# Kernel tuning notes

Measured on AMD Instinct MI355X. Metric: run time of the kernel, lower is better.

## Reference

```python
import jax, jax.numpy as jnp
import numpy as np
import math

TOP_K = 10  # top-k codes kept by SOHO_Pre_VD for negative sampling
EPS_LN = 1e-5


def layer_norm(x, w, b):
    mu = jnp.mean(x, axis=-1, keepdims=True)
    var = jnp.mean((x - mu) ** 2, axis=-1, keepdims=True)
    return (x - mu) * jax.lax.rsqrt(var + EPS_LN) * w + b


def position_encoding_sine(b, l, d):
    # mask is all-ones [b, l]; identical across batch, compute once and broadcast
    h = w = int(math.sqrt(l))
    ones = jnp.ones((h, w), jnp.float32)
    y_embed = jnp.cumsum(ones, axis=0)
    x_embed = jnp.cumsum(ones, axis=1)
    eps = 1e-6
    two_pi = 2.0 * np.pi
    y_embed = y_embed / (y_embed[-1:, :] + eps) * two_pi
    x_embed = x_embed / (x_embed[:, -1:] + eps) * two_pi
    pf = d // 2
    dim_t = jnp.arange(pf, dtype=jnp.float32)
    dim_t = 10000.0 ** (2.0 * jnp.floor(dim_t / 2.0) / pf)
    px = x_embed[:, :, None] / dim_t  # [h, w, pf]
    py = y_embed[:, :, None] / dim_t
    # interleave sin(even), cos(odd)
    px = jnp.stack([jnp.sin(px[..., 0::2]), jnp.cos(px[..., 1::2])], axis=-1).reshape(h, w, pf)
    py = jnp.stack([jnp.sin(py[..., 0::2]), jnp.cos(py[..., 1::2])], axis=-1).reshape(h, w, pf)
    pos = jnp.concatenate([py, px], axis=-1).reshape(l, d)  # [l, d]
    return jnp.broadcast_to(pos, (b, l, d))


def setup_inputs() -> dict:
    key = jax.random.key(0)
    ks = jax.random.split(key, 10)
    B, L, CIN, D, K = 16, 576, 1024, 768, 8192
    s = 0.02
    return {
        "img": jax.random.normal(ks[0], (B, L, CIN), jnp.float32),
        "mask_indices": jax.random.randint(ks[1], (B, 1), 0, L),
        "lin_w": jax.random.normal(ks[2], (D, CIN), jnp.float32) * s,
        "lin_b": jnp.zeros((D,), jnp.float32),
        "ln1_w": jnp.ones((D,), jnp.float32),
        "ln1_b": jnp.zeros((D,), jnp.float32),
        "embed": jax.random.normal(ks[3], (K, D), jnp.float32),
        "pos_w": jax.random.normal(ks[4], (D, D), jnp.float32) * s,
        "pos_b": jnp.zeros((D,), jnp.float32),
        "gate_w": jax.random.normal(ks[5], (2, 2 * D), jnp.float32) * s,
        "gate_b": jnp.zeros((2,), jnp.float32),
        "gate_ln_w": jnp.ones((2,), jnp.float32),
        "gate_ln_b": jnp.zeros((2,), jnp.float32),
        "out_ln_w": jnp.ones((D,), jnp.float32),
        "out_ln_b": jnp.zeros((D,), jnp.float32),
    }


def reference(img, mask_indices, lin_w, lin_b, ln1_w, ln1_b, embed, pos_w, pos_b,
              gate_w, gate_b, gate_ln_w, gate_ln_b, out_ln_w, out_ln_b):
    b, l, _ = img.shape
    d = lin_w.shape[0]
    # self.linear: Linear -> LayerNorm -> ReLU
    xq = jax.nn.relu(layer_norm(img @ lin_w.T + lin_b, ln1_w, ln1_b))  # [b,l,d]
    x = xq.reshape(b * l, d)
    # SOHO VQ: nearest code by L2, straight-through
    d2 = (x * x).sum(-1, keepdims=True) - 2.0 * (x @ embed.T) + (embed * embed).sum(-1)  # [N,K]
    idx = jnp.argmin(d2, axis=-1)  # [N]
    quant = jnp.take(embed, idx, axis=0)
    quantized = x + jax.lax.stop_gradient(quant - x)
    probs = jax.nn.softmax(-d2, axis=-1)
    topk_values, topk_indices = jax.lax.top_k(probs, TOP_K)  # [N,K'],[N,K']
    # pos_align linear
    quantized = quantized @ pos_w.T + pos_b
    emb_pt = quantized.reshape(b, l, d)
    # gated fusion
    g = jnp.concatenate([emb_pt, xq], axis=-1) @ gate_w.T + gate_b  # [b,l,2]
    g = jax.nn.relu(layer_norm(g, gate_ln_w, gate_ln_b))
    score = jax.nn.softmax(g, axis=-1)
    emb_s, img_s = score[..., 0:1], score[..., 1:2]
    emb_pt = emb_pt * emb_s + xq * img_s
    pos = position_encoding_sine(b, l, d)
    # negative index construction (visual_mask is all ones)
    ind = idx.reshape(b, l).astype(jnp.float32)  # [b,l]
    masked_labels = jnp.take_along_axis(ind, mask_indices, axis=1)  # [b,1]
    masked_neg = (ind == masked_labels).astype(jnp.float32)[..., None]  # [b,l,1]
    samp = jax.random.categorical(jax.random.key(42), jnp.log(topk_values))  # [N]
    neg = jnp.take_along_axis(topk_indices, samp[:, None], axis=1).reshape(b, l, 1).astype(jnp.float32)
    neg_at_mask = jnp.take_along_axis(neg[..., 0], mask_indices, axis=1)[..., None]  # [b,1,1]
    neg_idx = neg_at_mask * masked_neg + ind[..., None] * (1.0 - masked_neg)  # [b,l,1]
    neg_idx = neg_idx.reshape(b * l).astype(jnp.int32)
    # one-hot matmul == embedding gather
    neg_q = jnp.take(embed, neg_idx, axis=0).reshape(b, l, d)
    neg_q = neg_q * emb_s + jax.lax.stop_gradient(xq) * img_s
    out_pos = layer_norm(emb_pt + pos, out_ln_w, out_ln_b)
    out_neg = layer_norm(neg_q + pos, out_ln_w, out_ln_b)
    return (out_pos, out_neg)
```

## Files before the change

kernel.cpp:

```cpp
#include <hip/hip_runtime.h>
#include <stdint.h>

#define M_TOT  9216
#define D_     768
#define CIN_   1024
#define KCODE  8192
#define TOPK   10

typedef unsigned short u16;
typedef __bf16 bf16x8 __attribute__((ext_vector_type(8)));
typedef float f32x4 __attribute__((ext_vector_type(4)));


__device__ inline float block_sum(float v, float* red) {
    int t = threadIdx.x;
    red[t] = v;
    __syncthreads();
    #pragma unroll
    for (int s = 128; s > 0; s >>= 1) {
        if (t < s) red[t] += red[t + s];
        __syncthreads();
    }
    float r = red[0];
    __syncthreads();
    return r;
}

__device__ inline unsigned long long umin64(unsigned long long a, unsigned long long b) {
    return (a < b) ? a : b;
}

__device__ inline u16 f2bf(float f) {
    uint32_t u = __float_as_uint(f);
    uint32_t r = (u + 0x7fffu + ((u >> 16) & 1u)) >> 16;
    return (u16)r;
}
__device__ inline float bf2f(u16 h) {
    return __uint_as_float(((uint32_t)h) << 16);
}

__device__ inline unsigned long long shfl_xor_u64(unsigned long long v, int mask) {
    int lo = (int)(uint32_t)v, hi = (int)(uint32_t)(v >> 32);
    lo = __shfl_xor(lo, mask, 64);
    hi = __shfl_xor(hi, mask, 64);
    return ((unsigned long long)(uint32_t)hi << 32) | (uint32_t)lo;
}

#define GLDS(gp, lp) __builtin_amdgcn_global_load_lds( \
    (const __attribute__((address_space(1))) unsigned int*)(gp), \
    (__attribute__((address_space(3))) unsigned int*)(lp), 16, 0, 0)

__global__ __launch_bounds__(256) void k_split3(const float* __restrict__ in,
    u16* __restrict__ h, u16* __restrict__ m, u16* __restrict__ l, int n4)
{
    int i = blockIdx.x * 256 + threadIdx.x;
    int stride = gridDim.x * 256;
    for (; i < n4; i += stride) {
        float4 v = ((const float4*)in)[i];
        ushort4 hv, mv, lv;
        float x, r;
        x = v.x; hv.x = f2bf(x); r = x - bf2f(hv.x); mv.x = f2bf(r); lv.x = f2bf(r - bf2f(mv.x));
        x = v.y; hv.y = f2bf(x); r = x - bf2f(hv.y); mv.y = f2bf(r); lv.y = f2bf(r - bf2f(mv.y));
        x = v.z; hv.z = f2bf(x); r = x - bf2f(hv.z); mv.z = f2bf(r); lv.z = f2bf(r - bf2f(mv.z));
        x = v.w; hv.w = f2bf(x); r = x - bf2f(hv.w); mv.w = f2bf(r); lv.w = f2bf(r - bf2f(mv.w));
        ((ushort4*)h)[i] = hv; ((ushort4*)m)[i] = mv; ((ushort4*)l)[i] = lv;
    }
}

__global__ __launch_bounds__(256) void k_split2(const float* __restrict__ in,
    u16* __restrict__ h, u16* __restrict__ l, int n4)
{
    int i = blockIdx.x * 256 + threadIdx.x;
    int stride = gridDim.x * 256;
    for (; i < n4; i += stride) {
        float4 v = ((const float4*)in)[i];
        ushort4 hv, lv;
        hv.x = f2bf(v.x); lv.x = f2bf(v.x - bf2f(hv.x));
        hv.y = f2bf(v.y); lv.y = f2bf(v.y - bf2f(hv.y));
        hv.z = f2bf(v.z); lv.z = f2bf(v.z - bf2f(hv.z));
        hv.w = f2bf(v.w); lv.w = f2bf(v.w - bf2f(hv.w));
        ((ushort4*)h)[i] = hv; ((ushort4*)l)[i] = lv;
    }
}

__global__ __launch_bounds__(256) void k_gemm1_mfma(
    const u16* __restrict__ Ah, const u16* __restrict__ Am, const u16* __restrict__ Al,
    const u16* __restrict__ Bh, const u16* __restrict__ Bm, const u16* __restrict__ Bl,
    const float* __restrict__ bias, float* __restrict__ C)
{
    __shared__ __align__(16) u16 sm[24576];
    const int t = threadIdx.x;
    const int lane = t & 63, wid = t >> 6;
    const int row0 = blockIdx.y * 128, col0 = blockIdx.x * 128;
    const int r16 = lane & 15, kb = lane >> 4;
    const int wr = wid >> 1, wc = wid & 1;
    const int sc = (lane & 3) * 8;
    const int lrow = lane >> 2;

    f32x4 acc[4][4];
    #pragma unroll
    for (int mf = 0; mf < 4; ++mf)
        #pragma unroll
        for (int nf = 0; nf < 4; ++nf)
            acc[mf][nf] = (f32x4){0.f, 0.f, 0.f, 0.f};

    for (int k0 = 0; k0 < CIN_; k0 += 32) {
        __syncthreads();
        #pragma unroll
        for (int i = 0; i < 12; ++i) {
            int mat = i >> 1;
            int c = (i & 1) ? wid + 4 : wid;
            const u16* mp = (mat == 0) ? Ah : (mat == 1) ? Am : (mat == 2) ? Al
                          : (mat == 3) ? Bh : (mat == 4) ? Bm : Bl;
            int rbase = (mat < 3) ? row0 : col0;
            const u16* g = mp + (size_t)(rbase + c * 16 + lrow) * CIN_ + k0 + sc;
            GLDS(g, sm + mat * 4096 + c * 512);
        }
        __syncthreads();

        bf16x8 bh[4], bm[4], bl[4];
        #pragma unroll
        for (int nf = 0; nf < 4; ++nf) {
            int offb = 12288 + (wc * 64 + nf * 16 + r16) * 32 + kb * 8;
            bh[nf] = *(const bf16x8*)(sm + offb);
            bm[nf] = *(const bf16x8*)(sm + offb + 4096);
            bl[nf] = *(const bf16x8*)(sm + offb + 8192);
        }
        #pragma unroll
        for (int mf = 0; mf < 4; ++mf) {
            int offa = (wr * 64 + mf * 16 + r16) * 32 + kb * 8;
            bf16x8 ah = *(const bf16x8*)(sm + offa);
            bf16x8 am = *(const bf16x8*)(sm + offa + 4096);
            bf16x8 al = *(const bf16x8*)(sm + offa + 8192);
            #pragma unroll
            for (int nf = 0; nf < 4; ++nf) {
                acc[mf][nf] = __builtin_amdgcn_mfma_f32_16x16x32_bf16(ah, bh[nf], acc[mf][nf], 0, 0, 0);
                acc[mf][nf] = __builtin_amdgcn_mfma_f32_16x16x32_bf16(ah, bm[nf], acc[mf][nf], 0, 0, 0);
                acc[mf][nf] = __builtin_amdgcn_mfma_f32_16x16x32_bf16(am, bh[nf], acc[mf][nf], 0, 0, 0);
                acc[mf][nf] = __builtin_amdgcn_mfma_f32_16x16x32_bf16(am, bm[nf], acc[mf][nf], 0, 0, 0);
                acc[mf][nf] = __builtin_amdgcn_mfma_f32_16x16x32_bf16(ah, bl[nf], acc[mf][nf], 0, 0, 0);
                acc[mf][nf] = __builtin_amdgcn_mfma_f32_16x16x32_bf16(al, bh[nf], acc[mf][nf], 0, 0, 0);
            }
        }
    }

    #pragma unroll
    for (int mf = 0; mf < 4; ++mf) {
        #pragma unroll
        for (int q = 0; q < 4; ++q) {
            int m = row0 + wr * 64 + mf * 16 + kb * 4 + q;
            #pragma unroll
            for (int nf = 0; nf < 4; ++nf) {
                int n = col0 + wc * 64 + nf * 16 + r16;
                C[(size_t)m * D_ + n] = acc[mf][nf][q] + bias[n];
            }
        }
    }
}

__global__ __launch_bounds__(256) void k_gemm3_mfma(
    const u16* __restrict__ Eh, const u16* __restrict__ El,
    const u16* __restrict__ Ph, const u16* __restrict__ Pl,
    const int* __restrict__ gather,
    const float* __restrict__ bias, float* __restrict__ C)
{
    __shared__ __align__(16) u16 sm[16384];
    const int t = threadIdx.x;
    const int lane = t & 63, wid = t >> 6;
    const int row0 = blockIdx.y * 128, col0 = blockIdx.x * 128;
    const int r16 = lane & 15, kb = lane >> 4;
    const int wr = wid >> 1, wc = wid & 1;
    const int sc = (lane & 3) * 8;
    const int lrow = lane >> 2;

    int gi0 = gather[row0 + wid * 16 + lrow];
    int gi1 = gather[row0 + (wid + 4) * 16 + lrow];

    f32x4 acc[4][4];
    #pragma unroll
    for (int mf = 0; mf < 4; ++mf)
        #pragma unroll
        for (int nf = 0; nf < 4; ++nf)
            acc[mf][nf] = (f32x4){0.f, 0.f, 0.f, 0.f};

    for (int k0 = 0; k0 < D_; k0 += 32) {
        __syncthreads();
        #pragma unroll
        for (int i = 0; i < 8; ++i) {
            int mat = i >> 1;
            int c = (i & 1) ? wid + 4 : wid;
            int grow = (i & 1) ? gi1 : gi0;
            const u16* g;
            if (mat == 0)      g = Eh + (size_t)grow * D_ + k0 + sc;
            else if (mat == 1) g = El + (size_t)grow * D_ + k0 + sc;
            else if (mat == 2) g = Ph + (size_t)(col0 + c * 16 + lrow) * D_ + k0 + sc;
            else               g = Pl + (size_t)(col0 + c * 16 + lrow) * D_ + k0 + sc;
            GLDS(g, sm + mat * 4096 + c * 512);
        }
        __syncthreads();

        bf16x8 bh[4], bl[4];
        #pragma unroll
        for (int nf = 0; nf < 4; ++nf) {
            int offb = 8192 + (wc * 64 + nf * 16 + r16) * 32 + kb * 8;
            bh[nf] = *(const bf16x8*)(sm + offb);
            bl[nf] = *(const bf16x8*)(sm + offb + 4096);
        }
        #pragma unroll
        for (int mf = 0; mf < 4; ++mf) {
            int offa = (wr * 64 + mf * 16 + r16) * 32 + kb * 8;
            bf16x8 ah = *(const bf16x8*)(sm + offa);
            bf16x8 al = *(const bf16x8*)(sm + offa + 4096);
            #pragma unroll
            for (int nf = 0; nf < 4; ++nf) {
                acc[mf][nf] = __builtin_amdgcn_mfma_f32_16x16x32_bf16(ah, bh[nf], acc[mf][nf], 0, 0, 0);
                acc[mf][nf] = __builtin_amdgcn_mfma_f32_16x16x32_bf16(ah, bl[nf], acc[mf][nf], 0, 0, 0);
                acc[mf][nf] = __builtin_amdgcn_mfma_f32_16x16x32_bf16(al, bh[nf], acc[mf][nf], 0, 0, 0);
            }
        }
    }

    #pragma unroll
    for (int mf = 0; mf < 4; ++mf) {
        #pragma unroll
        for (int q = 0; q < 4; ++q) {
            int m = row0 + wr * 64 + mf * 16 + kb * 4 + q;
            #pragma unroll
            for (int nf = 0; nf < 4; ++nf) {
                int n = col0 + wc * 64 + nf * 16 + r16;
                C[(size_t)m * D_ + n] = acc[mf][nf][q] + bias[n];
            }
        }
    }
}

__global__ __launch_bounds__(256) void k_gemm2_mfma(
    const u16* __restrict__ Xh, const u16* __restrict__ Xl,
    const u16* __restrict__ Eh, const u16* __restrict__ El,
    const float* __restrict__ xsq, const float* __restrict__ esq,
    unsigned long long* __restrict__ amin)
{
    __shared__ __align__(16) u16 sm[16384];
    const int t = threadIdx.x;
    const int lane = t & 63, wid = t >> 6;
    const int row0 = blockIdx.y * 128, col0 = blockIdx.x * 128;
    const int r16 = lane & 15, kb = lane >> 4;
    const int wr = wid >> 1, wc = wid & 1;

    f32x4 acc[4][4];
    #pragma unroll
    for (int mf = 0; mf < 4; ++mf)
        #pragma unroll
        for (int nf = 0; nf < 4; ++nf)
            acc[mf][nf] = (f32x4){0.f, 0.f, 0.f, 0.f};

    const u16* sb = (wid == 0) ? Xh : (wid == 1) ? Xl : (wid == 2) ? Eh : El;
    const int rbase = (wid < 2) ? row0 : col0;
    const int srow = rbase + (lane >> 2);
    const int scol = (lane & 3) * 8;
    u16* ldsw = sm + wid * 4096;

    for (int k0 = 0; k0 < D_; k0 += 32) {
        __syncthreads();
        #pragma unroll
        for (int c = 0; c < 8; ++c) {
            const u16* g = sb + (size_t)(srow + c * 16) * D_ + k0 + scol;
            GLDS(g, ldsw + c * 512);
        }
        __syncthreads();

        bf16x8 bh[4], bl[4];
        #pragma unroll
        for (int nf = 0; nf < 4; ++nf) {
            int offb = 8192 + (wc * 64 + nf * 16 + r16) * 32 + kb * 8;
            bh[nf] = *(const bf16x8*)(sm + offb);
            bl[nf] = *(const bf16x8*)(sm + offb + 4096);
        }
        #pragma unroll
        for (int mf = 0; mf < 4; ++mf) {
            int offa = (wr * 64 + mf * 16 + r16) * 32 + kb * 8;
            bf16x8 ah = *(const bf16x8*)(sm + offa);
            bf16x8 al = *(const bf16x8*)(sm + offa + 4096);
            #pragma unroll
            for (int nf = 0; nf < 4; ++nf) {
                acc[mf][nf] = __builtin_amdgcn_mfma_f32_16x16x32_bf16(ah, bh[nf], acc[mf][nf], 0, 0, 0);
                acc[mf][nf] = __builtin_amdgcn_mfma_f32_16x16x32_bf16(ah, bl[nf], acc[mf][nf], 0, 0, 0);
                acc[mf][nf] = __builtin_amdgcn_mfma_f32_16x16x32_bf16(al, bh[nf], acc[mf][nf], 0, 0, 0);
            }
        }
    }

    float esqv[4];
    #pragma unroll
    for (int nf = 0; nf < 4; ++nf)
        esqv[nf] = esq[col0 + wc * 64 + nf * 16 + r16];

    #pragma unroll
    for (int mf = 0; mf < 4; ++mf) {
        #pragma unroll
        for (int q = 0; q < 4; ++q) {
            int m = row0 + wr * 64 + mf * 16 + kb * 4 + q;
            float xsv = xsq[m];
            unsigned long long best = ~0ull;
            #pragma unroll
            for (int nf = 0; nf < 4; ++nf) {
                int n = col0 + wc * 64 + nf * 16 + r16;
                float d2 = (xsv - 2.0f * acc[mf][nf][q]) + esqv[nf];
                unsigned long long key =
                    ((unsigned long long)__float_as_uint(d2) << 32) | (unsigned)n;
                best = umin64(best, key);
            }
            #pragma unroll
            for (int msk = 1; msk < 16; msk <<= 1)
                best = umin64(best, shfl_xor_u64(best, msk));
            if (r16 == 0) atomicMin(&amin[m], best);
        }
    }
}

__global__ __launch_bounds__(256) void k_ln_relu(
    const float* __restrict__ in, const float* __restrict__ w,
    const float* __restrict__ b, float* __restrict__ xq, float* __restrict__ xsq,
    u16* __restrict__ Xh, u16* __restrict__ Xl)
{
    __shared__ float red[256];
    int r = blockIdx.x, t = threadIdx.x;
    const float* row = in + (size_t)r * D_;
    float v0 = row[t], v1 = row[t + 256], v2 = row[t + 512];
    float mu = block_sum(v0 + v1 + v2, red) * (1.0f / 768.0f);
    float d0 = v0 - mu, d1 = v1 - mu, d2 = v2 - mu;
    float var = block_sum(d0 * d0 + d1 * d1 + d2 * d2, red) * (1.0f / 768.0f);
    float rn = 1.0f / sqrtf(var + 1e-5f);
    float o0 = fmaxf(0.0f, d0 * rn * w[t] + b[t]);
    float o1 = fmaxf(0.0f, d1 * rn * w[t + 256] + b[t + 256]);
    float o2 = fmaxf(0.0f, d2 * rn * w[t + 512] + b[t + 512]);
    float* orow = xq + (size_t)r * D_;
    orow[t] = o0; orow[t + 256] = o1; orow[t + 512] = o2;
    u16 h0 = f2bf(o0), h1 = f2bf(o1), h2 = f2bf(o2);
    Xh[(size_t)r * D_ + t]       = h0;
    Xh[(size_t)r * D_ + t + 256] = h1;
    Xh[(size_t)r * D_ + t + 512] = h2;
    Xl[(size_t)r * D_ + t]       = f2bf(o0 - bf2f(h0));
    Xl[(size_t)r * D_ + t + 256] = f2bf(o1 - bf2f(h1));
    Xl[(size_t)r * D_ + t + 512] = f2bf(o2 - bf2f(h2));
    float q = block_sum(o0 * o0 + o1 * o1 + o2 * o2, red);
    if (t == 0) xsq[r] = q;
}

__global__ __launch_bounds__(256) void k_esq(const float* __restrict__ E,
                                             float* __restrict__ esq,
                                             u16* __restrict__ Eh,
                                             u16* __restrict__ El)
{
    __shared__ float red[256];
    int r = blockIdx.x, t = threadIdx.x;
    const float* row = E + (size_t)r * D_;
    float v0 = row[t], v1 = row[t + 256], v2 = row[t + 512];
    u16 h0 = f2bf(v0), h1 = f2bf(v1), h2 = f2bf(v2);
    Eh[(size_t)r * D_ + t]       = h0;
    Eh[(size_t)r * D_ + t + 256] = h1;
    Eh[(size_t)r * D_ + t + 512] = h2;
    El[(size_t)r * D_ + t]       = f2bf(v0 - bf2f(h0));
    El[(size_t)r * D_ + t + 256] = f2bf(v1 - bf2f(h1));
    El[(size_t)r * D_ + t + 512] = f2bf(v2 - bf2f(h2));
    float s = block_sum(v0 * v0 + v1 * v1 + v2 * v2, red);
    if (t == 0) esq[r] = s;
}

__global__ void k_extract(const unsigned long long* __restrict__ amin,
                          int* __restrict__ idx, int n)
{
    int i = blockIdx.x * 256 + threadIdx.x;
    if (i < n) idx[i] = (int)(amin[i] & 0xFFFFFFFFull);
}

__global__ __launch_bounds__(256) void k_gate(
    const float* __restrict__ embpt, const float* __restrict__ xq,
    const float* __restrict__ gw, const float* __restrict__ gb,
    const float* __restrict__ glnw, const float* __restrict__ glnb,
    float* __restrict__ scores)
{
    __shared__ float red[256];
    int r = blockIdx.x, t = threadIdx.x;
    const float* ep = embpt + (size_t)r * D_;
    const float* xr = xq + (size_t)r * D_;
    float g0 = 0.0f, g1 = 0.0f;
    for (int k = t; k < 1536; k += 256) {
        float v = (k < 768) ? ep[k] : xr[k - 768];
        g0 = fmaf(v, gw[k], g0);
        g1 = fmaf(v, gw[1536 + k], g1);
    }
    g0 = block_sum(g0, red);
    g1 = block_sum(g1, red);
    if (t == 0) {
        g0 += gb[0]; g1 += gb[1];
        float mu = 0.5f * (g0 + g1);
        float h0 = g0 - mu, h1 = g1 - mu;
        float var = 0.5f * (h0 * h0 + h1 * h1);
        float rn = 1.0f / sqrtf(var + 1e-5f);
        float o0 = fmaxf(0.0f, h0 * rn * glnw[0] + glnb[0]);
        float o1 = fmaxf(0.0f, h1 * rn * glnw[1] + glnb[1]);
        float m = fmaxf(o0, o1);
        float e0 = expf(o0 - m), e1 = expf(o1 - m);
        float inv = 1.0f / (e0 + e1);
        scores[r * 2 + 0] = e0 * inv;
        scores[r * 2 + 1] = e1 * inv;
    }
}

__global__ __launch_bounds__(256) void k_pos(float* __restrict__ pos)
{
    int l = blockIdx.x, t = threadIdx.x;
    for (int k = t; k < D_; k += 256) {
        int kk = (k < 384) ? k : k - 384;
        int m = kk >> 1;
        double coord = (k < 384) ? (double)(l / 24) : (double)(l % 24);
        double v = (coord + 1.0) / (24.0 + 1e-6) * 6.283185307179586;
        double tm = pow(10000.0, (double)m / 192.0);
        double a = v / tm;
        pos[(size_t)l * D_ + k] = (float)((kk & 1) ? cos(a) : sin(a));
    }
}

__global__ __launch_bounds__(256) void k_d2row(
    const float* __restrict__ xq, const float* __restrict__ E,
    const float* __restrict__ xsq, const float* __restrict__ esq,
    const int* __restrict__ mask, float* __restrict__ d2row)
{
    __shared__ float xs[768];
    int b = blockIdx.x;
    int g = blockIdx.y;
    int t = threadIdx.x;
    int r = b * 576 + mask[b];
    xs[t]       = xq[(size_t)r * D_ + t];
    xs[t + 256] = xq[(size_t)r * D_ + t + 256];
    xs[t + 512] = xq[(size_t)r * D_ + t + 512];
    __syncthreads();
    int lane = t & 63, w = t >> 6;
    float xsr = xsq[r];
    for (int e = 0; e < 16; ++e) {
        int j = g * 64 + w * 16 + e;
        const float* er = E + (size_t)j * D_;
        float p = 0.0f;
        for (int k = lane; k < D_; k += 64) p = fmaf(xs[k], er[k], p);
        #pragma unroll
        for (int off = 32; off > 0; off >>= 1) p += __shfl_down(p, off);
        if (lane == 0) d2row[b * KCODE + j] = (xsr - 2.0f * p) + esq[j];
    }
}

__device__ inline void threefry2x32(uint32_t x0, uint32_t x1,
                                    uint32_t& o0, uint32_t& o1)
{
    const uint32_t ks0 = 0u, ks1 = 42u;
    const uint32_t ks2 = ks0 ^ ks1 ^ 0x1BD11BDAu;
    uint32_t ks[3] = {ks0, ks1, ks2};
    x0 += ks[0]; x1 += ks[1];
    const int R0[4] = {13, 15, 26, 6};
    const int R1[4] = {17, 29, 16, 24};
    #pragma unroll
    for (int i = 0; i < 5; ++i) {
        const int* R = (i & 1) ? R1 : R0;
        #pragma unroll
        for (int q = 0; q < 4; ++q) {
            x0 += x1;
            x1 = (x1 << R[q]) | (x1 >> (32 - R[q]));
            x1 ^= x0;
        }
        x0 += ks[(i + 1) % 3];
        x1 += ks[(i + 2) % 3] + (uint32_t)(i + 1);
    }
    o0 = x0; o1 = x1;
}

__global__ __launch_bounds__(256) void k_topk_sample(
    const float* __restrict__ d2row, const unsigned long long* __restrict__ amin,
    const int* __restrict__ mask, int* __restrict__ mlabel, int* __restrict__ negsel)
{
    __shared__ float sd2[KCODE];
    __shared__ unsigned long long rbuf[256];
    __shared__ float rfs[256];
    __shared__ int sel[TOPK];
    __shared__ float selv[TOPK];
    __shared__ float sS;
    int b = blockIdx.x, t = threadIdx.x;
    for (int j = t; j < KCODE; j += 256) sd2[j] = d2row[b * KCODE + j];
    __syncthreads();
    for (int p = 0; p < TOPK; ++p) {
        unsigned long long best = ~0ull;
        for (int j = t; j < KCODE; j += 256) {
            bool skip = false;
            for (int q = 0; q < p; ++q) skip = skip || (j == sel[q]);
            if (skip) continue;
            unsigned long long key =
                ((unsigned long long)__float_as_uint(sd2[j]) << 32) | (unsigned)j;
            best = umin64(best, key);
        }
        rbuf[t] = best;
        __syncthreads();
        for (int s = 128; s > 0; s >>= 1) {
            if (t < s) rbuf[t] = umin64(rbuf[t], rbuf[t + s]);
            __syncthreads();
        }
// ... 160 lines not shown
```

Before: 880.5 us.

## Double-buffer LDS staging in split-bf16 GEMMs and switch to k-major LDS layout

The gather-GEMM and distance-GEMM kernels now use two LDS buffers, prefetching the next K tile with global_load_lds while MFMAs run on the current one. This leaves one barrier per iteration instead of two. The LDS layout of all three GEMMs changes to k-major chunks, with each lane loading a full row segment, to change access and bank patterns. The positional-encoding kernel replaces double-precision pow/sin/cos with float exp2f/sinf/cosf, trading some accuracy for cheaper math. Double buffering doubles shared memory per block, which may reduce occupancy.

```diff
diff --git a/kernel.cpp b/kernel.cpp
--- a/kernel.cpp
+++ b/kernel.cpp
@@ -50,38 +50,6 @@
     (const __attribute__((address_space(1))) unsigned int*)(gp), \
     (__attribute__((address_space(3))) unsigned int*)(lp), 16, 0, 0)
 
-__global__ __launch_bounds__(256) void k_split3(const float* __restrict__ in,
-    u16* __restrict__ h, u16* __restrict__ m, u16* __restrict__ l, int n4)
-{
-    int i = blockIdx.x * 256 + threadIdx.x;
-    int stride = gridDim.x * 256;
-    for (; i < n4; i += stride) {
-        float4 v = ((const float4*)in)[i];
-        ushort4 hv, mv, lv;
-        float x, r;
-        x = v.x; hv.x = f2bf(x); r = x - bf2f(hv.x); mv.x = f2bf(r); lv.x = f2bf(r - bf2f(mv.x));
-        x = v.y; hv.y = f2bf(x); r = x - bf2f(hv.y); mv.y = f2bf(r); lv.y = f2bf(r - bf2f(mv.y));
-        x = v.z; hv.z = f2bf(x); r = x - bf2f(hv.z); mv.z = f2bf(r); lv.z = f2bf(r - bf2f(mv.z));
-        x = v.w; hv.w = f2bf(x); r = x - bf2f(hv.w); mv.w = f2bf(r); lv.w = f2bf(r - bf2f(mv.w));
-        ((ushort4*)h)[i] = hv; ((ushort4*)m)[i] = mv; ((ushort4*)l)[i] = lv;
-    }
-}
-
-__global__ __launch_bounds__(256) void k_split2(const float* __restrict__ in,
-    u16* __restrict__ h, u16* __restrict__ l, int n4)
-{
-    int i = blockIdx.x * 256 + threadIdx.x;
-    int stride = gridDim.x * 256;
-    for (; i < n4; i += stride) {
-        float4 v = ((const float4*)in)[i];
-        ushort4 hv, lv;
-        hv.x = f2bf(v.x); lv.x = f2bf(v.x - bf2f(hv.x));
-        hv.y = f2bf(v.y); lv.y = f2bf(v.y - bf2f(hv.y));
-        hv.z = f2bf(v.z); lv.z = f2bf(v.z - bf2f(hv.z));
-        hv.w = f2bf(v.w); lv.w = f2bf(v.w - bf2f(hv.w));
-        ((ushort4*)h)[i] = hv; ((ushort4*)l)[i] = lv;
-    }
-}
 
 __global__ __launch_bounds__(256) void k_gemm1_mfma(
     const u16* __restrict__ Ah, const u16* __restrict__ Am, const u16* __restrict__ Al,
@@ -94,8 +62,6 @@
     const int row0 = blockIdx.y * 128, col0 = blockIdx.x * 128;
     const int r16 = lane & 15, kb = lane >> 4;
     const int wr = wid >> 1, wc = wid & 1;
-    const int sc = (lane & 3) * 8;
-    const int lrow = lane >> 2;
 
     f32x4 acc[4][4];
     #pragma unroll
@@ -113,7 +79,8 @@
             const u16* mp = (mat == 0) ? Ah : (mat == 1) ? Am : (mat == 2) ? Al
                           : (mat == 3) ? Bh : (mat == 4) ? Bm : Bl;
             int rbase = (mat < 3) ? row0 : col0;
-            const u16* g = mp + (size_t)(rbase + c * 16 + lrow) * CIN_ + k0 + sc;
+            const u16* g = mp + (size_t)(rbase + (c & 1) * 64 + lane) * CIN_
+                             + k0 + (c >> 1) * 8;
             GLDS(g, sm + mat * 4096 + c * 512);
         }
         __syncthreads();
@@ -121,17 +88,17 @@
         bf16x8 bh[4], bm[4], bl[4];
         #pragma unroll
         for (int nf = 0; nf < 4; ++nf) {
-            int offb = 12288 + (wc * 64 + nf * 16 + r16) * 32 + kb * 8;
-            bh[nf] = *(const bf16x8*)(sm + offb);
-            bm[nf] = *(const bf16x8*)(sm + offb + 4096);
-            bl[nf] = *(const bf16x8*)(sm + offb + 8192);
+            int off = kb * 1024 + (wc * 64 + nf * 16 + r16) * 8;
+            bh[nf] = *(const bf16x8*)(sm + 12288 + off);
+            bm[nf] = *(const bf16x8*)(sm + 16384 + off);
+            bl[nf] = *(const bf16x8*)(sm + 20480 + off);
         }
         #pragma unroll
         for (int mf = 0; mf < 4; ++mf) {
-            int offa = (wr * 64 + mf * 16 + r16) * 32 + kb * 8;
-            bf16x8 ah = *(const bf16x8*)(sm + offa);
-            bf16x8 am = *(const bf16x8*)(sm + offa + 4096);
-            bf16x8 al = *(const bf16x8*)(sm + offa + 8192);
+            int off = kb * 1024 + (wr * 64 + mf * 16 + r16) * 8;
+            bf16x8 ah = *(const bf16x8*)(sm + off);
+            bf16x8 am = *(const bf16x8*)(sm + 4096 + off);
+            bf16x8 al = *(const bf16x8*)(sm + 8192 + off);
             #pragma unroll
             for (int nf = 0; nf < 4; ++nf) {
                 acc[mf][nf] = __builtin_amdgcn_mfma_f32_16x16x32_bf16(ah, bh[nf], acc[mf][nf], 0, 0, 0);
@@ -164,17 +131,12 @@
     const int* __restrict__ gather,
     const float* __restrict__ bias, float* __restrict__ C)
 {
-    __shared__ __align__(16) u16 sm[16384];
+    __shared__ __align__(16) u16 sm[2][16384];
     const int t = threadIdx.x;
     const int lane = t & 63, wid = t >> 6;
     const int row0 = blockIdx.y * 128, col0 = blockIdx.x * 128;
     const int r16 = lane & 15, kb = lane >> 4;
     const int wr = wid >> 1, wc = wid & 1;
-    const int sc = (lane & 3) * 8;
-    const int lrow = lane >> 2;
-
-    int gi0 = gather[row0 + wid * 16 + lrow];
-    int gi1 = gather[row0 + (wid + 4) * 16 + lrow];
 
     f32x4 acc[4][4];
     #pragma unroll
@@ -183,34 +145,45 @@
         for (int nf = 0; nf < 4; ++nf)
             acc[mf][nf] = (f32x4){0.f, 0.f, 0.f, 0.f};
 
-    for (int k0 = 0; k0 < D_; k0 += 32) {
-        __syncthreads();
-        #pragma unroll
-        for (int i = 0; i < 8; ++i) {
-            int mat = i >> 1;
-            int c = (i & 1) ? wid + 4 : wid;
-            int grow = (i & 1) ? gi1 : gi0;
-            const u16* g;
-            if (mat == 0)      g = Eh + (size_t)grow * D_ + k0 + sc;
-            else if (mat == 1) g = El + (size_t)grow * D_ + k0 + sc;
-            else if (mat == 2) g = Ph + (size_t)(col0 + c * 16 + lrow) * D_ + k0 + sc;
-            else               g = Pl + (size_t)(col0 + c * 16 + lrow) * D_ + k0 + sc;
-            GLDS(g, sm + mat * 4096 + c * 512);
-        }
-        __syncthreads();
-
+    const u16* sb = (wid == 0) ? Eh : (wid == 1) ? El : (wid == 2) ? Ph : Pl;
+    int re, ro;
+    if (wid < 2) {
+        re = gather[row0 + lane];
+        ro = gather[row0 + 64 + lane];
+    } else {
+        re = col0 + lane;
+        ro = col0 + 64 + lane;
+    }
+    const u16* src0 = sb + (size_t)re * D_;
+    const u16* src1 = sb + (size_t)ro * D_;
+
+    auto STAGE = [&](int buf, int k0) {
+        u16* dst = sm[buf] + wid * 4096;
+        #pragma unroll
+        for (int c = 0; c < 8; ++c) {
+            const u16* g = ((c & 1) ? src1 : src0) + k0 + (c >> 1) * 8;
+            GLDS(g, dst + c * 512);
+        }
+    };
+
+    STAGE(0, 0);
+    __syncthreads();
+    for (int kt = 0; kt < 24; ++kt) {
+        int cur = kt & 1;
+        if (kt < 23) STAGE(cur ^ 1, (kt + 1) * 32);
+        const u16* B = sm[cur];
         bf16x8 bh[4], bl[4];
         #pragma unroll
         for (int nf = 0; nf < 4; ++nf) {
-            int offb = 8192 + (wc * 64 + nf * 16 + r16) * 32 + kb * 8;
-            bh[nf] = *(const bf16x8*)(sm + offb);
-            bl[nf] = *(const bf16x8*)(sm + offb + 4096);
+            int off = kb * 1024 + (wc * 64 + nf * 16 + r16) * 8;
+            bh[nf] = *(const bf16x8*)(B + 8192 + off);
+            bl[nf] = *(const bf16x8*)(B + 12288 + off);
         }
         #pragma unroll
         for (int mf = 0; mf < 4; ++mf) {
-            int offa = (wr * 64 + mf * 16 + r16) * 32 + kb * 8;
-            bf16x8 ah = *(const bf16x8*)(sm + offa);
-            bf16x8 al = *(const bf16x8*)(sm + offa + 4096);
+            int off = kb * 1024 + (wr * 64 + mf * 16 + r16) * 8;
+            bf16x8 ah = *(const bf16x8*)(B + off);
+            bf16x8 al = *(const bf16x8*)(B + 4096 + off);
             #pragma unroll
             for (int nf = 0; nf < 4; ++nf) {
                 acc[mf][nf] = __builtin_amdgcn_mfma_f32_16x16x32_bf16(ah, bh[nf], acc[mf][nf], 0, 0, 0);
@@ -218,6 +191,7 @@
                 acc[mf][nf] = __builtin_amdgcn_mfma_f32_16x16x32_bf16(al, bh[nf], acc[mf][nf], 0, 0, 0);
             }
         }
+        __syncthreads();
     }
 
     #pragma unroll
@@ -240,7 +214,7 @@
     const float* __restrict__ xsq, const float* __restrict__ esq,
     unsigned long long* __restrict__ amin)
 {
-    __shared__ __align__(16) u16 sm[16384];
+    __shared__ __align__(16) u16 sm[2][16384];
     const int t = threadIdx.x;
     const int lane = t & 63, wid = t >> 6;
     const int row0 = blockIdx.y * 128, col0 = blockIdx.x * 128;
@@ -256,31 +230,36 @@
 
     const u16* sb = (wid == 0) ? Xh : (wid == 1) ? Xl : (wid == 2) ? Eh : El;
     const int rbase = (wid < 2) ? row0 : col0;
-    const int srow = rbase + (lane >> 2);
-    const int scol = (lane & 3) * 8;
-    u16* ldsw = sm + wid * 4096;
-
-    for (int k0 = 0; k0 < D_; k0 += 32) {
-        __syncthreads();
+    const u16* src0 = sb + (size_t)(rbase + lane) * D_;
+    const u16* src1 = sb + (size_t)(rbase + 64 + lane) * D_;
+
+    auto STAGE = [&](int buf, int k0) {
+        u16* dst = sm[buf] + wid * 4096;
         #pragma unroll
         for (int c = 0; c < 8; ++c) {
-            const u16* g = sb + (size_t)(srow + c * 16) * D_ + k0 + scol;
-            GLDS(g, ldsw + c * 512);
-        }
-        __syncthreads();
-
+            const u16* g = ((c & 1) ? src1 : src0) + k0 + (c >> 1) * 8;
+            GLDS(g, dst + c * 512);
+        }
+    };
+
+    STAGE(0, 0);
+    __syncthreads();
+    for (int kt = 0; kt < 24; ++kt) {
+        int cur = kt & 1;
+        if (kt < 23) STAGE(cur ^ 1, (kt + 1) * 32);
+        const u16* B = sm[cur];
         bf16x8 bh[4], bl[4];
         #pragma unroll
         for (int nf = 0; nf < 4; ++nf) {
-            int offb = 8192 + (wc * 64 + nf * 16 + r16) * 32 + kb * 8;
-            bh[nf] = *(const bf16x8*)(sm + offb);
-            bl[nf] = *(const bf16x8*)(sm + offb + 4096);
+            int off = kb * 1024 + (wc * 64 + nf * 16 + r16) * 8;
+            bh[nf] = *(const bf16x8*)(B + 8192 + off);
+            bl[nf] = *(const bf16x8*)(B + 12288 + off);
         }
         #pragma unroll
         for (int mf = 0; mf < 4; ++mf) {
-            int offa = (wr * 64 + mf * 16 + r16) * 32 + kb * 8;
-            bf16x8 ah = *(const bf16x8*)(sm + offa);
-            bf16x8 al = *(const bf16x8*)(sm + offa + 4096);
+            int off = kb * 1024 + (wr * 64 + mf * 16 + r16) * 8;
+            bf16x8 ah = *(const bf16x8*)(B + off);
+            bf16x8 al = *(const bf16x8*)(B + 4096 + off);
             #pragma unroll
             for (int nf = 0; nf < 4; ++nf) {
                 acc[mf][nf] = __builtin_amdgcn_mfma_f32_16x16x32_bf16(ah, bh[nf], acc[mf][nf], 0, 0, 0);
@@ -288,6 +267,7 @@
                 acc[mf][nf] = __builtin_amdgcn_mfma_f32_16x16x32_bf16(al, bh[nf], acc[mf][nf], 0, 0, 0);
             }
         }
+        __syncthreads();
     }
 
     float esqv[4];
@@ -315,6 +295,39 @@
                 best = umin64(best, shfl_xor_u64(best, msk));
             if (r16 == 0) atomicMin(&amin[m], best);
         }
+    }
+}
+
+__global__ __launch_bounds__(256) void k_split3(const float* __restrict__ in,
+    u16* __restrict__ h, u16* __restrict__ m, u16* __restrict__ l, int n4)
+{
+    int i = blockIdx.x * 256 + threadIdx.x;
+    int stride = gridDim.x * 256;
+    for (; i < n4; i += stride) {
+        float4 v = ((const float4*)in)[i];
+        ushort4 hv, mv, lv;
+        float x, r;
+        x = v.x; hv.x = f2bf(x); r = x - bf2f(hv.x); mv.x = f2bf(r); lv.x = f2bf(r - bf2f(mv.x));
+        x = v.y; hv.y = f2bf(x); r = x - bf2f(hv.y); mv.y = f2bf(r); lv.y = f2bf(r - bf2f(mv.y));
+        x = v.z; hv.z = f2bf(x); r = x - bf2f(hv.z); mv.z = f2bf(r); lv.z = f2bf(r - bf2f(mv.z));
+        x = v.w; hv.w = f2bf(x); r = x - bf2f(hv.w); mv.w = f2bf(r); lv.w = f2bf(r - bf2f(mv.w));
+        ((ushort4*)h)[i] = hv; ((ushort4*)m)[i] = mv; ((ushort4*)l)[i] = lv;
+    }
+}
+
+__global__ __launch_bounds__(256) void k_split2(const float* __restrict__ in,
+    u16* __restrict__ h, u16* __restrict__ l, int n4)
+{
+    int i = blockIdx.x * 256 + threadIdx.x;
+    int stride = gridDim.x * 256;
+    for (; i < n4; i += stride) {
+        float4 v = ((const float4*)in)[i];
+        ushort4 hv, lv;
+        hv.x = f2bf(v.x); lv.x = f2bf(v.x - bf2f(hv.x));
+        hv.y = f2bf(v.y); lv.y = f2bf(v.y - bf2f(hv.y));
+        hv.z = f2bf(v.z); lv.z = f2bf(v.z - bf2f(hv.z));
+        hv.w = f2bf(v.w); lv.w = f2bf(v.w - bf2f(hv.w));
+        ((ushort4*)h)[i] = hv; ((ushort4*)l)[i] = lv;
     }
 }
 
@@ -414,11 +427,11 @@
     for (int k = t; k < D_; k += 256) {
         int kk = (k < 384) ? k : k - 384;
         int m = kk >> 1;
-        double coord = (k < 384) ? (double)(l / 24) : (double)(l % 24);
-        double v = (coord + 1.0) / (24.0 + 1e-6) * 6.283185307179586;
-        double tm = pow(10000.0, (double)m / 192.0);
-        double a = v / tm;
-        pos[(size_t)l * D_ + k] = (float)((kk & 1) ? cos(a) : sin(a));
+        float coord = (k < 384) ? (float)(l / 24) : (float)(l % 24);
+        float v = (coord + 1.0f) / 24.000001f * 6.28318530717958647692f;
+        float tm = exp2f((float)m * (13.287712379549449f / 192.0f));
+        float a = v / tm;
+        pos[(size_t)l * D_ + k] = (kk & 1) ? cosf(a) : sinf(a);
     }
 }
 
```

New measurement: 1.463 ms. 1.66x slower.

## Widen gemm2 K-tile to 64 with XOR-swizzled LDS and float pos encoding

Applied to the files above, without the earlier changes.

The distance GEMM kernel now stages 64-wide K slices instead of 32, in a 32K-element shared buffer. It uses an XOR-swizzled LDS layout to avoid bank conflicts and halves the number of barrier pairs per tile. The kernel definitions are also moved earlier in the file. Separately, the sine position encoding switches from double-precision pow/sin/cos to float exp2f/sinf/cosf. That is cheaper on the GPU but slightly less accurate.

```diff
diff --git a/kernel.cpp b/kernel.cpp
--- a/kernel.cpp
+++ b/kernel.cpp
@@ -49,6 +49,244 @@
 #define GLDS(gp, lp) __builtin_amdgcn_global_load_lds( \
     (const __attribute__((address_space(1))) unsigned int*)(gp), \
     (__attribute__((address_space(3))) unsigned int*)(lp), 16, 0, 0)
+
+__global__ __launch_bounds__(256) void k_gemm1_mfma(
+    const u16* __restrict__ Ah, const u16* __restrict__ Am, const u16* __restrict__ Al,
+    const u16* __restrict__ Bh, const u16* __restrict__ Bm, const u16* __restrict__ Bl,
+    const float* __restrict__ bias, float* __restrict__ C)
+{
+    __shared__ __align__(16) u16 sm[24576];
+    const int t = threadIdx.x;
+    const int lane = t & 63, wid = t >> 6;
+    const int row0 = blockIdx.y * 128, col0 = blockIdx.x * 128;
+    const int r16 = lane & 15, kb = lane >> 4;
+    const int wr = wid >> 1, wc = wid & 1;
+    const int sc = (lane & 3) * 8;
+    const int lrow = lane >> 2;
+
+    f32x4 acc[4][4];
+    #pragma unroll
+    for (int mf = 0; mf < 4; ++mf)
+        #pragma unroll
+        for (int nf = 0; nf < 4; ++nf)
+            acc[mf][nf] = (f32x4){0.f, 0.f, 0.f, 0.f};
+
+    for (int k0 = 0; k0 < CIN_; k0 += 32) {
+        __syncthreads();
+        #pragma unroll
+        for (int i = 0; i < 12; ++i) {
+            int mat = i >> 1;
+            int c = (i & 1) ? wid + 4 : wid;
+            const u16* mp = (mat == 0) ? Ah : (mat == 1) ? Am : (mat == 2) ? Al
+                          : (mat == 3) ? Bh : (mat == 4) ? Bm : Bl;
+            int rbase = (mat < 3) ? row0 : col0;
+            const u16* g = mp + (size_t)(rbase + c * 16 + lrow) * CIN_ + k0 + sc;
+            GLDS(g, sm + mat * 4096 + c * 512);
+        }
+        __syncthreads();
+
+        bf16x8 bh[4], bm[4], bl[4];
+        #pragma unroll
+        for (int nf = 0; nf < 4; ++nf) {
+            int offb = 12288 + (wc * 64 + nf * 16 + r16) * 32 + kb * 8;
+            bh[nf] = *(const bf16x8*)(sm + offb);
+            bm[nf] = *(const bf16x8*)(sm + offb + 4096);
+            bl[nf] = *(const bf16x8*)(sm + offb + 8192);
+        }
+        #pragma unroll
+        for (int mf = 0; mf < 4; ++mf) {
+            int offa = (wr * 64 + mf * 16 + r16) * 32 + kb * 8;
+            bf16x8 ah = *(const bf16x8*)(sm + offa);
+            bf16x8 am = *(const bf16x8*)(sm + offa + 4096);
+            bf16x8 al = *(const bf16x8*)(sm + offa + 8192);
+            #pragma unroll
+            for (int nf = 0; nf < 4; ++nf) {
+                acc[mf][nf] = __builtin_amdgcn_mfma_f32_16x16x32_bf16(ah, bh[nf], acc[mf][nf], 0, 0, 0);
+                acc[mf][nf] = __builtin_amdgcn_mfma_f32_16x16x32_bf16(ah, bm[nf], acc[mf][nf], 0, 0, 0);
+                acc[mf][nf] = __builtin_amdgcn_mfma_f32_16x16x32_bf16(am, bh[nf], acc[mf][nf], 0, 0, 0);
+                acc[mf][nf] = __builtin_amdgcn_mfma_f32_16x16x32_bf16(am, bm[nf], acc[mf][nf], 0, 0, 0);
+                acc[mf][nf] = __builtin_amdgcn_mfma_f32_16x16x32_bf16(ah, bl[nf], acc[mf][nf], 0, 0, 0);
+                acc[mf][nf] = __builtin_amdgcn_mfma_f32_16x16x32_bf16(al, bh[nf], acc[mf][nf], 0, 0, 0);
+            }
+        }
+    }
+
+    #pragma unroll
+    for (int mf = 0; mf < 4; ++mf) {
+        #pragma unroll
+        for (int q = 0; q < 4; ++q) {
+            int m = row0 + wr * 64 + mf * 16 + kb * 4 + q;
+            #pragma unroll
+            for (int nf = 0; nf < 4; ++nf) {
+                int n = col0 + wc * 64 + nf * 16 + r16;
+                C[(size_t)m * D_ + n] = acc[mf][nf][q] + bias[n];
+            }
+        }
+    }
+}
+
+__global__ __launch_bounds__(256) void k_gemm3_mfma(
+    const u16* __restrict__ Eh, const u16* __restrict__ El,
+    const u16* __restrict__ Ph, const u16* __restrict__ Pl,
+    const int* __restrict__ gather,
+    const float* __restrict__ bias, float* __restrict__ C)
+{
+    __shared__ __align__(16) u16 sm[16384];
+    const int t = threadIdx.x;
+    const int lane = t & 63, wid = t >> 6;
+    const int row0 = blockIdx.y * 128, col0 = blockIdx.x * 128;
+    const int r16 = lane & 15, kb = lane >> 4;
+    const int wr = wid >> 1, wc = wid & 1;
+    const int sc = (lane & 3) * 8;
+    const int lrow = lane >> 2;
+
+    int gi0 = gather[row0 + wid * 16 + lrow];
+    int gi1 = gather[row0 + (wid + 4) * 16 + lrow];
+
+    f32x4 acc[4][4];
+    #pragma unroll
+    for (int mf = 0; mf < 4; ++mf)
+        #pragma unroll
+        for (int nf = 0; nf < 4; ++nf)
+            acc[mf][nf] = (f32x4){0.f, 0.f, 0.f, 0.f};
+
+    for (int k0 = 0; k0 < D_; k0 += 32) {
+        __syncthreads();
+        #pragma unroll
+        for (int i = 0; i < 8; ++i) {
+            int mat = i >> 1;
+            int c = (i & 1) ? wid + 4 : wid;
+            int grow = (i & 1) ? gi1 : gi0;
+            const u16* g;
+            if (mat == 0)      g = Eh + (size_t)grow * D_ + k0 + sc;
+            else if (mat == 1) g = El + (size_t)grow * D_ + k0 + sc;
+            else if (mat == 2) g = Ph + (size_t)(col0 + c * 16 + lrow) * D_ + k0 + sc;
+            else               g = Pl + (size_t)(col0 + c * 16 + lrow) * D_ + k0 + sc;
+            GLDS(g, sm + mat * 4096 + c * 512);
+        }
+        __syncthreads();
+
+        bf16x8 bh[4], bl[4];
+        #pragma unroll
+        for (int nf = 0; nf < 4; ++nf) {
+            int offb = 8192 + (wc * 64 + nf * 16 + r16) * 32 + kb * 8;
+            bh[nf] = *(const bf16x8*)(sm + offb);
+            bl[nf] = *(const bf16x8*)(sm + offb + 4096);
+        }
+        #pragma unroll
+        for (int mf = 0; mf < 4; ++mf) {
+            int offa = (wr * 64 + mf * 16 + r16) * 32 + kb * 8;
+            bf16x8 ah = *(const bf16x8*)(sm + offa);
+            bf16x8 al = *(const bf16x8*)(sm + offa + 4096);
+            #pragma unroll
+            for (int nf = 0; nf < 4; ++nf) {
+                acc[mf][nf] = __builtin_amdgcn_mfma_f32_16x16x32_bf16(ah, bh[nf], acc[mf][nf], 0, 0, 0);
+                acc[mf][nf] = __builtin_amdgcn_mfma_f32_16x16x32_bf16(ah, bl[nf], acc[mf][nf], 0, 0, 0);
+                acc[mf][nf] = __builtin_amdgcn_mfma_f32_16x16x32_bf16(al, bh[nf], acc[mf][nf], 0, 0, 0);
+            }
+        }
+    }
+
+    #pragma unroll
+    for (int mf = 0; mf < 4; ++mf) {
+        #pragma unroll
+        for (int q = 0; q < 4; ++q) {
+            int m = row0 + wr * 64 + mf * 16 + kb * 4 + q;
+            #pragma unroll
+            for (int nf = 0; nf < 4; ++nf) {
+                int n = col0 + wc * 64 + nf * 16 + r16;
+                C[(size_t)m * D_ + n] = acc[mf][nf][q] + bias[n];
+            }
+        }
+    }
+}
+
+__global__ __launch_bounds__(256) void k_gemm2_mfma(
+    const u16* __restrict__ Xh, const u16* __restrict__ Xl,
+    const u16* __restrict__ Eh, const u16* __restrict__ El,
+    const float* __restrict__ xsq, const float* __restrict__ esq,
+    unsigned long long* __restrict__ amin)
+{
+    __shared__ __align__(16) u16 sm[32768];
+    const int t = threadIdx.x;
+    const int lane = t & 63, wid = t >> 6;
+    const int row0 = blockIdx.y * 128, col0 = blockIdx.x * 128;
+    const int r16 = lane & 15, kb = lane >> 4;
+    const int wr = wid >> 1, wc = wid & 1;
+
+    f32x4 acc[4][4];
+    #pragma unroll
+    for (int mf = 0; mf < 4; ++mf)
+        #pragma unroll
+        for (int nf = 0; nf < 4; ++nf)
+            acc[mf][nf] = (f32x4){0.f, 0.f, 0.f, 0.f};
+
+    const u16* sb = (wid == 0) ? Xh : (wid == 1) ? Xl : (wid == 2) ? Eh : El;
+    const int rbase = (wid < 2) ? row0 : col0;
+    const u16* srcb = sb + (size_t)(rbase + (lane >> 3)) * D_
+                         + ((lane & 7) ^ (lane >> 3)) * 8;
+    u16* dstb = sm + wid * 8192 + lane * 8;
+
+    const int swz = (r16 & 7);
+    for (int kt = 0; kt < 12; ++kt) {
+        __syncthreads();
+        #pragma unroll
+        for (int c = 0; c < 16; ++c) {
+            GLDS(srcb + kt * 64 + c * 8 * D_, dstb + c * 512);
+        }
+        __syncthreads();
+        #pragma unroll
+        for (int h = 0; h < 2; ++h) {
+            const int slot = ((h * 4 + kb) ^ swz) * 8;
+            bf16x8 bh[4], bl[4];
+            #pragma unroll
+            for (int nf = 0; nf < 4; ++nf) {
+                int off = (wc * 64 + nf * 16 + r16) * 64 + slot;
+                bh[nf] = *(const bf16x8*)(sm + 16384 + off);
+                bl[nf] = *(const bf16x8*)(sm + 24576 + off);
+            }
+            #pragma unroll
+            for (int mf = 0; mf < 4; ++mf) {
+                int off = (wr * 64 + mf * 16 + r16) * 64 + slot;
+                bf16x8 ah = *(const bf16x8*)(sm + off);
+                bf16x8 al = *(const bf16x8*)(sm + 8192 + off);
+                #pragma unroll
+                for (int nf = 0; nf < 4; ++nf) {
+                    acc[mf][nf] = __builtin_amdgcn_mfma_f32_16x16x32_bf16(ah, bh[nf], acc[mf][nf], 0, 0, 0);
+                    acc[mf][nf] = __builtin_amdgcn_mfma_f32_16x16x32_bf16(ah, bl[nf], acc[mf][nf], 0, 0, 0);
+                    acc[mf][nf] = __builtin_amdgcn_mfma_f32_16x16x32_bf16(al, bh[nf], acc[mf][nf], 0, 0, 0);
+                }
+            }
+        }
+    }
+
+    float esqv[4];
+    #pragma unroll
+    for (int nf = 0; nf < 4; ++nf)
+        esqv[nf] = esq[col0 + wc * 64 + nf * 16 + r16];
+
+    #pragma unroll
+    for (int mf = 0; mf < 4; ++mf) {
+        #pragma unroll
+        for (int q = 0; q < 4; ++q) {
+            int m = row0 + wr * 64 + mf * 16 + kb * 4 + q;
+            float xsv = xsq[m];
+            unsigned long long best = ~0ull;
+            #pragma unroll
+            for (int nf = 0; nf < 4; ++nf) {
+                int n = col0 + wc * 64 + nf * 16 + r16;
+                float d2 = (xsv - 2.0f * acc[mf][nf][q]) + esqv[nf];
+                unsigned long long key =
+                    ((unsigned long long)__float_as_uint(d2) << 32) | (unsigned)n;
+                best = umin64(best, key);
+            }
+            #pragma unroll
+            for (int msk = 1; msk < 16; msk <<= 1)
+                best = umin64(best, shfl_xor_u64(best, msk));
+            if (r16 == 0) atomicMin(&amin[m], best);
+        }
+    }
+}
 
 __global__ __launch_bounds__(256) void k_split3(const float* __restrict__ in,
     u16* __restrict__ h, u16* __restrict__ m, u16* __restrict__ l, int n4)
@@ -80,241 +318,6 @@
         hv.z = f2bf(v.z); lv.z = f2bf(v.z - bf2f(hv.z));
         hv.w = f2bf(v.w); lv.w = f2bf(v.w - bf2f(hv.w));
         ((ushort4*)h)[i] = hv; ((ushort4*)l)[i] = lv;
-    }
-}
-
-__global__ __launch_bounds__(256) void k_gemm1_mfma(
-    const u16* __restrict__ Ah, const u16* __restrict__ Am, const u16* __restrict__ Al,
-    const u16* __restrict__ Bh, const u16* __restrict__ Bm, const u16* __restrict__ Bl,
-    const float* __restrict__ bias, float* __restrict__ C)
-{
-    __shared__ __align__(16) u16 sm[24576];
-    const int t = threadIdx.x;
-    const int lane = t & 63, wid = t >> 6;
-    const int row0 = blockIdx.y * 128, col0 = blockIdx.x * 128;
-    const int r16 = lane & 15, kb = lane >> 4;
-    const int wr = wid >> 1, wc = wid & 1;
-    const int sc = (lane & 3) * 8;
-    const int lrow = lane >> 2;
-
-    f32x4 acc[4][4];
-    #pragma unroll
-    for (int mf = 0; mf < 4; ++mf)
-        #pragma unroll
-        for (int nf = 0; nf < 4; ++nf)
-            acc[mf][nf] = (f32x4){0.f, 0.f, 0.f, 0.f};
-
-    for (int k0 = 0; k0 < CIN_; k0 += 32) {
-        __syncthreads();
-        #pragma unroll
-        for (int i = 0; i < 12; ++i) {
-            int mat = i >> 1;
-            int c = (i & 1) ? wid + 4 : wid;
-            const u16* mp = (mat == 0) ? Ah : (mat == 1) ? Am : (mat == 2) ? Al
-                          : (mat == 3) ? Bh : (mat == 4) ? Bm : Bl;
-            int rbase = (mat < 3) ? row0 : col0;
-            const u16* g = mp + (size_t)(rbase + c * 16 + lrow) * CIN_ + k0 + sc;
-            GLDS(g, sm + mat * 4096 + c * 512);
-        }
-        __syncthreads();
-
-        bf16x8 bh[4], bm[4], bl[4];
-        #pragma unroll
-        for (int nf = 0; nf < 4; ++nf) {
-            int offb = 12288 + (wc * 64 + nf * 16 + r16) * 32 + kb * 8;
-            bh[nf] = *(const bf16x8*)(sm + offb);
-            bm[nf] = *(const bf16x8*)(sm + offb + 4096);
-            bl[nf] = *(const bf16x8*)(sm + offb + 8192);
-        }
-        #pragma unroll
-        for (int mf = 0; mf < 4; ++mf) {
-            int offa = (wr * 64 + mf * 16 + r16) * 32 + kb * 8;
-            bf16x8 ah = *(const bf16x8*)(sm + offa);
-            bf16x8 am = *(const bf16x8*)(sm + offa + 4096);
-            bf16x8 al = *(const bf16x8*)(sm + offa + 8192);
-            #pragma unroll
-            for (int nf = 0; nf < 4; ++nf) {
-                acc[mf][nf] = __builtin_amdgcn_mfma_f32_16x16x32_bf16(ah, bh[nf], acc[mf][nf], 0, 0, 0);
-                acc[mf][nf] = __builtin_amdgcn_mfma_f32_16x16x32_bf16(ah, bm[nf], acc[mf][nf], 0, 0, 0);
-                acc[mf][nf] = __builtin_amdgcn_mfma_f32_16x16x32_bf16(am, bh[nf], acc[mf][nf], 0, 0, 0);
-                acc[mf][nf] = __builtin_amdgcn_mfma_f32_16x16x32_bf16(am, bm[nf], acc[mf][nf], 0, 0, 0);
-                acc[mf][nf] = __builtin_amdgcn_mfma_f32_16x16x32_bf16(ah, bl[nf], acc[mf][nf], 0, 0, 0);
-                acc[mf][nf] = __builtin_amdgcn_mfma_f32_16x16x32_bf16(al, bh[nf], acc[mf][nf], 0, 0, 0);
-            }
-        }
-    }
-
-    #pragma unroll
-    for (int mf = 0; mf < 4; ++mf) {
-        #pragma unroll
-        for (int q = 0; q < 4; ++q) {
-            int m = row0 + wr * 64 + mf * 16 + kb * 4 + q;
-            #pragma unroll
-            for (int nf = 0; nf < 4; ++nf) {
-                int n = col0 + wc * 64 + nf * 16 + r16;
-                C[(size_t)m * D_ + n] = acc[mf][nf][q] + bias[n];
-            }
-        }
-    }
-}
-
-__global__ __launch_bounds__(256) void k_gemm3_mfma(
-    const u16* __restrict__ Eh, const u16* __restrict__ El,
-    const u16* __restrict__ Ph, const u16* __restrict__ Pl,
-    const int* __restrict__ gather,
-    const float* __restrict__ bias, float* __restrict__ C)
-{
-    __shared__ __align__(16) u16 sm[16384];
-    const int t = threadIdx.x;
-    const int lane = t & 63, wid = t >> 6;
-    const int row0 = blockIdx.y * 128, col0 = blockIdx.x * 128;
-    const int r16 = lane & 15, kb = lane >> 4;
-    const int wr = wid >> 1, wc = wid & 1;
-    const int sc = (lane & 3) * 8;
-    const int lrow = lane >> 2;
-
-    int gi0 = gather[row0 + wid * 16 + lrow];
-    int gi1 = gather[row0 + (wid + 4) * 16 + lrow];
-
-    f32x4 acc[4][4];
-    #pragma unroll
-    for (int mf = 0; mf < 4; ++mf)
-        #pragma unroll
-        for (int nf = 0; nf < 4; ++nf)
-            acc[mf][nf] = (f32x4){0.f, 0.f, 0.f, 0.f};
-
-    for (int k0 = 0; k0 < D_; k0 += 32) {
-        __syncthreads();
-        #pragma unroll
-        for (int i = 0; i < 8; ++i) {
-            int mat = i >> 1;
-            int c = (i & 1) ? wid + 4 : wid;
-            int grow = (i & 1) ? gi1 : gi0;
-            const u16* g;
-            if (mat == 0)      g = Eh + (size_t)grow * D_ + k0 + sc;
-            else if (mat == 1) g = El + (size_t)grow * D_ + k0 + sc;
-            else if (mat == 2) g = Ph + (size_t)(col0 + c * 16 + lrow) * D_ + k0 + sc;
-            else               g = Pl + (size_t)(col0 + c * 16 + lrow) * D_ + k0 + sc;
-            GLDS(g, sm + mat * 4096 + c * 512);
-        }
-        __syncthreads();
-
-        bf16x8 bh[4], bl[4];
-        #pragma unroll
-        for (int nf = 0; nf < 4; ++nf) {
-            int offb = 8192 + (wc * 64 + nf * 16 + r16) * 32 + kb * 8;
-            bh[nf] = *(const bf16x8*)(sm + offb);
-            bl[nf] = *(const bf16x8*)(sm + offb + 4096);
-        }
-        #pragma unroll
-        for (int mf = 0; mf < 4; ++mf) {
-            int offa = (wr * 64 + mf * 16 + r16) * 32 + kb * 8;
-            bf16x8 ah = *(const bf16x8*)(sm + offa);
-            bf16x8 al = *(const bf16x8*)(sm + offa + 4096);
-            #pragma unroll
-            for (int nf = 0; nf < 4; ++nf) {
-                acc[mf][nf] = __builtin_amdgcn_mfma_f32_16x16x32_bf16(ah, bh[nf], acc[mf][nf], 0, 0, 0);
-                acc[mf][nf] = __builtin_amdgcn_mfma_f32_16x16x32_bf16(ah, bl[nf], acc[mf][nf], 0, 0, 0);
-                acc[mf][nf] = __builtin_amdgcn_mfma_f32_16x16x32_bf16(al, bh[nf], acc[mf][nf], 0, 0, 0);
-            }
-        }
-    }
-
-    #pragma unroll
-    for (int mf = 0; mf < 4; ++mf) {
-        #pragma unroll
-        for (int q = 0; q < 4; ++q) {
-            int m = row0 + wr * 64 + mf * 16 + kb * 4 + q;
-            #pragma unroll
-            for (int nf = 0; nf < 4; ++nf) {
-                int n = col0 + wc * 64 + nf * 16 + r16;
-                C[(size_t)m * D_ + n] = acc[mf][nf][q] + bias[n];
-            }
-        }
-    }
-}
-
-__global__ __launch_bounds__(256) void k_gemm2_mfma(
-    const u16* __restrict__ Xh, const u16* __restrict__ Xl,
-    const u16* __restrict__ Eh, const u16* __restrict__ El,
-    const float* __restrict__ xsq, const float* __restrict__ esq,
-    unsigned long long* __restrict__ amin)
-{
-    __shared__ __align__(16) u16 sm[16384];
-    const int t = threadIdx.x;
-    const int lane = t & 63, wid = t >> 6;
-    const int row0 = blockIdx.y * 128, col0 = blockIdx.x * 128;
-    const int r16 = lane & 15, kb = lane >> 4;
-    const int wr = wid >> 1, wc = wid & 1;
-
-    f32x4 acc[4][4];
-    #pragma unroll
-    for (int mf = 0; mf < 4; ++mf)
-        #pragma unroll
-        for (int nf = 0; nf < 4; ++nf)
-            acc[mf][nf] = (f32x4){0.f, 0.f, 0.f, 0.f};
-
-    const u16* sb = (wid == 0) ? Xh : (wid == 1) ? Xl : (wid == 2) ? Eh : El;
-    const int rbase = (wid < 2) ? row0 : col0;
-    const int srow = rbase + (lane >> 2);
-    const int scol = (lane & 3) * 8;
-    u16* ldsw = sm + wid * 4096;
-
-    for (int k0 = 0; k0 < D_; k0 += 32) {
-        __syncthreads();
-        #pragma unroll
-        for (int c = 0; c < 8; ++c) {
-            const u16* g = sb + (size_t)(srow + c * 16) * D_ + k0 + scol;
-            GLDS(g, ldsw + c * 512);
-        }
-        __syncthreads();
-
-        bf16x8 bh[4], bl[4];
-        #pragma unroll
-        for (int nf = 0; nf < 4; ++nf) {
-            int offb = 8192 + (wc * 64 + nf * 16 + r16) * 32 + kb * 8;
-            bh[nf] = *(const bf16x8*)(sm + offb);
-            bl[nf] = *(const bf16x8*)(sm + offb + 4096);
-        }
-        #pragma unroll
-        for (int mf = 0; mf < 4; ++mf) {
-            int offa = (wr * 64 + mf * 16 + r16) * 32 + kb * 8;
-            bf16x8 ah = *(const bf16x8*)(sm + offa);
-            bf16x8 al = *(const bf16x8*)(sm + offa + 4096);
-            #pragma unroll
-            for (int nf = 0; nf < 4; ++nf) {
-                acc[mf][nf] = __builtin_amdgcn_mfma_f32_16x16x32_bf16(ah, bh[nf], acc[mf][nf], 0, 0, 0);
-                acc[mf][nf] = __builtin_amdgcn_mfma_f32_16x16x32_bf16(ah, bl[nf], acc[mf][nf], 0, 0, 0);
-                acc[mf][nf] = __builtin_amdgcn_mfma_f32_16x16x32_bf16(al, bh[nf], acc[mf][nf], 0, 0, 0);
-            }
-        }
-    }
-
-    float esqv[4];
-    #pragma unroll
-    for (int nf = 0; nf < 4; ++nf)
-        esqv[nf] = esq[col0 + wc * 64 + nf * 16 + r16];
-
-    #pragma unroll
-    for (int mf = 0; mf < 4; ++mf) {
-        #pragma unroll
-        for (int q = 0; q < 4; ++q) {
-            int m = row0 + wr * 64 + mf * 16 + kb * 4 + q;
-            float xsv = xsq[m];
-            unsigned long long best = ~0ull;
-            #pragma unroll
-            for (int nf = 0; nf < 4; ++nf) {
-                int n = col0 + wc * 64 + nf * 16 + r16;
-                float d2 = (xsv - 2.0f * acc[mf][nf][q]) + esqv[nf];
-                unsigned long long key =
-                    ((unsigned long long)__float_as_uint(d2) << 32) | (unsigned)n;
-                best = umin64(best, key);
-            }
-            #pragma unroll
-            for (int msk = 1; msk < 16; msk <<= 1)
-                best = umin64(best, shfl_xor_u64(best, msk));
-            if (r16 == 0) atomicMin(&amin[m], best);
-        }
     }
 }
 
@@ -414,11 +417,11 @@
     for (int k = t; k < D_; k += 256) {
         int kk = (k < 384) ? k : k - 384;
         int m = kk >> 1;
-        double coord = (k < 384) ? (double)(l / 24) : (double)(l % 24);
-        double v = (coord + 1.0) / (24.0 + 1e-6) * 6.283185307179586;
-        double tm = pow(10000.0, (double)m / 192.0);
-        double a = v / tm;
-        pos[(size_t)l * D_ + k] = (float)((kk & 1) ? cos(a) : sin(a));
+        float coord = (k < 384) ? (float)(l / 24) : (float)(l % 24);
+        float v = (coord + 1.0f) / 24.000001f * 6.28318530717958647692f;
+        float tm = exp2f((float)m * (13.287712379549449f / 192.0f));
+        float a = v / tm;
+        pos[(size_t)l * D_ + k] = (kk & 1) ? cosf(a) : sinf(a);
     }
 }
 
```

Result: faster. 818.7 us (-7.0%).
